# Optimization experiments

Measured on AMD Instinct MI355X. Metric: run time of the kernel, lower is better.

The kernel has to match this reference:

```python
import jax, jax.numpy as jnp
import numpy as np

EMBED = 1024
KEY = 64
HEAD = 64
CTX = 4096
BATCH = 8


def _linear(x, w, b):
    # torch nn.Linear: y = x @ W.T + b, W shape [out, in]
    return x @ w.T + b


def setup_inputs() -> dict:
    key = jax.random.key(0)
    ks = jax.random.split(key, 11)
    s_e = 1.0 / np.sqrt(EMBED)
    s_k = 1.0 / np.sqrt(KEY)
    return {
        "embeddings": jax.random.normal(ks[0], (BATCH, CTX, EMBED), dtype=jnp.float32),
        "kw1": jax.random.uniform(ks[1], (KEY, EMBED), jnp.float32, -s_e, s_e),
        "kb1": jax.random.uniform(ks[2], (KEY,), jnp.float32, -s_e, s_e),
        "kw2": jax.random.uniform(ks[3], (KEY, KEY), jnp.float32, -s_k, s_k),
        "kb2": jax.random.uniform(ks[4], (KEY,), jnp.float32, -s_k, s_k),
        "qw1": jax.random.uniform(ks[5], (KEY, EMBED), jnp.float32, -s_e, s_e),
        "qb1": jax.random.uniform(ks[6], (KEY,), jnp.float32, -s_e, s_e),
        "qw2": jax.random.uniform(ks[7], (KEY, KEY), jnp.float32, -s_k, s_k),
        "qb2": jax.random.uniform(ks[8], (KEY,), jnp.float32, -s_k, s_k),
        "vw": jax.random.uniform(ks[9], (HEAD, EMBED), jnp.float32, -s_e, s_e),
        "vb": jax.random.uniform(ks[10], (HEAD,), jnp.float32, -s_e, s_e),
    }


def reference(embeddings, kw1, kb1, kw2, kb2, qw1, qb1, qw2, qb2, vw, vb):
    T = embeddings.shape[1]
    keys = jax.nn.relu(_linear(jax.nn.relu(_linear(embeddings, kw1, kb1)), kw2, kb2))
    queries = jax.nn.relu(_linear(jax.nn.relu(_linear(embeddings, qw1, qb1)), qw2, qb2))
    values = _linear(embeddings, vw, vb)
    # scores: [B, T, T]
    scores = jnp.einsum("btk,bsk->bts", queries, keys) / np.sqrt(KEY).astype(np.float32)
    # Faithful to original: tril(ones) * -1e10 added (masks lower triangle incl. diagonal)
    mask = jnp.tril(jnp.ones((T, T), dtype=jnp.float32)) * jnp.float32(-1e10)
    weights = jax.nn.softmax(scores + mask, axis=-1)
    return jnp.einsum("bts,bsh->bth", weights, values)
```

## Files before the change

### kernel.cpp

```cpp
#include <hip/hip_runtime.h>
#include <hip/hip_bf16.h>
#include <math.h>

#define NB   8
#define TCTX 4096
#define ED   1024
#define KD   64

typedef __attribute__((ext_vector_type(8))) short bf16x8;
typedef __attribute__((ext_vector_type(4))) float f32x4;

#define LOG2E  1.44269504088896340736f
#define SCALE2 (0.125f * LOG2E)
#define MASK2  (-1e10f * LOG2E)

__device__ __forceinline__ void lds_fence() {
    asm volatile("s_waitcnt lgkmcnt(0)" ::: "memory");
    __builtin_amdgcn_sched_barrier(0);
}

__device__ __forceinline__ unsigned short f2bf(float f) {
    union { float f; unsigned u; } c; c.f = f;
    return (unsigned short)((c.u + 0x7FFFu + ((c.u >> 16) & 1u)) >> 16);
}
__device__ __forceinline__ int swz(int row, int byteoff) {
    return row * 128 + (byteoff ^ ((row & 7) << 4));
}
__device__ __forceinline__ f32x4 fzero4() {
    f32x4 z; z[0] = 0.f; z[1] = 0.f; z[2] = 0.f; z[3] = 0.f; return z;
}
__device__ __forceinline__ void gl_lds16(const void* g, void* l) {
    __builtin_amdgcn_global_load_lds(
        (const __attribute__((address_space(1))) unsigned int*)g,
        (__attribute__((address_space(3))) unsigned int*)l, 16, 0, 0);
}
__device__ __forceinline__ unsigned cvtpk_bf16(float lo, float hi) {
    unsigned r;
    asm("v_cvt_pk_bf16_f32 %0, %1, %2" : "=v"(r) : "v"(lo), "v"(hi));
    return r;
}

__global__ __launch_bounds__(256) void prep_kernel(
    const float* __restrict__ kw1, const float* __restrict__ qw1,
    const float* __restrict__ vw,  const float* __restrict__ kw2,
    const float* __restrict__ qw2,
    unsigned short* __restrict__ W1p, unsigned short* __restrict__ W2p)
{
    int idx = blockIdx.x * 256 + threadIdx.x;
    if (idx < 24576) {
        int ks = idx / 1536, rem = idx % 1536;
        int r = rem >> 3, bb = rem & 7;
        int c = bb ^ (r & 7);
        const float* src = (r < 64)  ? (kw1 + r * ED)
                         : (r < 128) ? (qw1 + (r - 64) * ED)
                                     : (vw  + (r - 128) * ED);
        src += ks * 64 + c * 8;
        unsigned short* dst = W1p + (size_t)idx * 8;
        #pragma unroll
        for (int e = 0; e < 8; ++e) dst[e] = f2bf(src[e]);
    } else if (idx < 25600) {
        int j = idx - 24576;
        int lane = j & 63, kh = (j >> 6) & 1, n = (j >> 7) & 3, kq = j >> 9;
        int row = n * 16 + (lane & 15);
        int ko  = kh * 32 + (lane >> 4) * 8;
        const float* src = (kq ? qw2 : kw2) + row * 64 + ko;
        unsigned short* dst = W2p + (size_t)j * 8;
        #pragma unroll
        for (int e = 0; e < 8; ++e) dst[e] = f2bf(src[e]);
    }
}

__global__ __launch_bounds__(256, 2) void proj_kernel(
    const float* __restrict__ emb,
    const unsigned short* __restrict__ W1p, const unsigned short* __restrict__ W2p,
    const float* __restrict__ kb1, const float* __restrict__ kb2,
    const float* __restrict__ qb1, const float* __restrict__ qb2,
    const float* __restrict__ vb,
    unsigned short* __restrict__ Qo, unsigned short* __restrict__ Ko,
    unsigned short* __restrict__ Vt)
{
    __shared__ __align__(16) char lds[80 * 1024];

    const int tid  = threadIdx.x;
    const int lane = tid & 63;
    const int w    = tid >> 6;
    const int lr   = lane & 15;
    const int lg   = lane >> 4;
    const long r0  = (long)blockIdx.x * 64;
    const int  b   = blockIdx.x >> 6;
    const int  tb  = (blockIdx.x & 63) * 64;

    const float* embB = emb + r0 * ED;

    f32x4 acc[12];
    #pragma unroll
    for (int j = 0; j < 12; ++j) acc[j] = fzero4();

    auto stageA = [&](int buf, int ks) {
        char* Abuf = lds + buf * 16 * 1024;
        const float* eb = embB + ks * 64;
        #pragma unroll
        for (int j = 0; j < 4; ++j) {
            int chunk = j * 4 + w;
            int r = chunk * 4 + (lane >> 4);
            int c = (lane & 15) ^ (r & 7);
            gl_lds16(eb + (long)r * ED + c * 4, Abuf + chunk * 1024);
        }
    };
    auto stageB = [&](int buf, int ks) {
        char* Bbuf = lds + 32 * 1024 + buf * 24 * 1024;
        const unsigned short* wb = W1p + (size_t)ks * 12288;
        #pragma unroll
        for (int j = 0; j < 6; ++j) {
            int chunk = j * 4 + w;
            gl_lds16(wb + chunk * 512 + lane * 8, Bbuf + chunk * 1024);
        }
    };

    stageA(0, 0); stageB(0, 0);
    __syncthreads();

    int cur = 0;
    for (int ks = 0; ks < 16; ++ks) {
        if (ks < 15) { stageA(cur ^ 1, ks + 1); stageB(cur ^ 1, ks + 1); }
        char* Ac = lds + cur * 16 * 1024;
        char* Bc = lds + 32 * 1024 + cur * 24 * 1024;
        const int r = w * 16 + lr;
        #pragma unroll
        for (int kh = 0; kh < 2; ++kh) {
            int cb0 = kh * 8 + lg * 2;
            float4 fa = *(const float4*)(Ac + r * 256 + ((cb0 ^ (r & 7)) * 16));
            float4 fb = *(const float4*)(Ac + r * 256 + (((cb0 + 1) ^ (r & 7)) * 16));
            bf16x8 a;
            a[0] = (short)f2bf(fa.x); a[1] = (short)f2bf(fa.y);
            a[2] = (short)f2bf(fa.z); a[3] = (short)f2bf(fa.w);
            a[4] = (short)f2bf(fb.x); a[5] = (short)f2bf(fb.y);
            a[6] = (short)f2bf(fb.z); a[7] = (short)f2bf(fb.w);
            #pragma unroll
            for (int n = 0; n < 12; ++n) {
                bf16x8 bv = *(const bf16x8*)(Bc + swz(n * 16 + lr, kh * 64 + lg * 16));
                acc[n] = __builtin_amdgcn_mfma_f32_16x16x32_bf16(a, bv, acc[n], 0, 0, 0);
            }
        }
        __syncthreads();
        cur ^= 1;
    }

    char* H  = lds + w * 2048;
    char* VT = lds + 16 * 1024;

    #pragma unroll
    for (int kq = 0; kq < 2; ++kq) {
        const float* b1 = kq ? qb1 : kb1;
        const float* b2 = kq ? qb2 : kb2;
        unsigned short* dst = kq ? Qo : Ko;
        const float oscale = kq ? SCALE2 : 1.0f;
        #pragma unroll
        for (int n = 0; n < 4; ++n) {
            int col = n * 16 + lr;
            float bias = b1[col];
            #pragma unroll
            for (int rr = 0; rr < 4; ++rr) {
                int row = lg * 4 + rr;
                *(unsigned short*)(H + swz(row, col * 2)) =
                    f2bf(fmaxf(acc[kq * 4 + n][rr] + bias, 0.f));
            }
        }
        lds_fence();
        bf16x8 a2k0 = *(const bf16x8*)(H + swz(lr, 0 * 64 + lg * 16));
        bf16x8 a2k1 = *(const bf16x8*)(H + swz(lr, 1 * 64 + lg * 16));
        lds_fence();

        f32x4 acc2[4];
        #pragma unroll
        for (int n = 0; n < 4; ++n) acc2[n] = fzero4();
        #pragma unroll
        for (int n = 0; n < 4; ++n) {
            bf16x8 w2f0 = *(const bf16x8*)(W2p + ((kq * 4 + n) * 2 + 0) * 512 + lane * 8);
            bf16x8 w2f1 = *(const bf16x8*)(W2p + ((kq * 4 + n) * 2 + 1) * 512 + lane * 8);
            acc2[n] = __builtin_amdgcn_mfma_f32_16x16x32_bf16(a2k0, w2f0, acc2[n], 0, 0, 0);
            acc2[n] = __builtin_amdgcn_mfma_f32_16x16x32_bf16(a2k1, w2f1, acc2[n], 0, 0, 0);
        }
        #pragma unroll
        for (int n = 0; n < 4; ++n) {
            int col = n * 16 + lr;
            float bias = b2[col];
            #pragma unroll
            for (int rr = 0; rr < 4; ++rr) {
                long rg = r0 + w * 16 + lg * 4 + rr;
                dst[rg * KD + col] = f2bf(fmaxf(acc2[n][rr] + bias, 0.f) * oscale);
            }
        }
    }

    #pragma unroll
    for (int n = 0; n < 4; ++n) {
        int col = n * 16 + lr;
        float bias = vb[col];
        #pragma unroll
        for (int rr = 0; rr < 4; ++rr) {
            int tl = w * 16 + lg * 4 + rr;
            *(unsigned short*)(VT + swz(col, tl * 2)) = f2bf(acc[8 + n][rr] + bias);
        }
    }
    __syncthreads();
    #pragma unroll
    for (int it = 0; it < 2; ++it) {
        int c = it * 256 + tid;
        int h = c >> 3, c4 = c & 7;
        *(int4*)(Vt + ((long)b * KD + h) * TCTX + tb + c4 * 8) =
            *(const int4*)(VT + swz(h, c4 * 16));
    }
}

__global__ __launch_bounds__(128) void attn_kernel(
    const unsigned short* __restrict__ Qb,
    const unsigned short* __restrict__ Kb,
    const unsigned short* __restrict__ Vt,
    float* __restrict__ Opart, float2* __restrict__ MSum)
{
    __shared__ __align__(16) char lds[20 * 1024];

    const int bid  = blockIdx.x;
    const int b    = bid & 7;
    const int half = (bid >> 3) & 1;
    const int qr   = bid >> 4;
    const int qi   = (qr + 127) & 127;
    const int t0   = qi * 32;
    const int tid = threadIdx.x, lane = tid & 63, w = tid >> 6;
    const int lr  = lane & 15, lg = lane >> 4;
    const int tg  = t0 + w * 16 + lr;

    char* Kl = lds;
    char* Vl = lds + 8 * 1024;
    char* QP = lds + 16 * 1024 + w * 2048;

    const unsigned short* Qg  = Qb + ((long)b * TCTX + t0 + w * 16) * KD;
    const unsigned short* Kg0 = Kb + (long)b * TCTX * KD;
    const unsigned short* Vg0 = Vt + (long)b * KD * TCTX;

    const int srow = lane >> 3;
    const int sblk = lane & 7;

    const int s0q = (qi == 127) ? 0 : (qi >> 1);
    const int len = 64 - s0q;
    const int mid = s0q + ((len + 1) >> 1);
    const int s_lo = half ? mid : s0q;
    const int s_hi = half ? 64  : mid;

    auto stageK = [&](int si) {
        const unsigned short* Kg = Kg0 + si * 64 * KD;
        #pragma unroll
        for (int j = 0; j < 4; ++j) {
            int chunk = w * 4 + j;
            int r = chunk * 8 + srow;
            int c = sblk ^ (r & 7);
            gl_lds16(Kg + r * KD + c * 8, Kl + chunk * 1024);
        }
    };
    auto stageV = [&](int si) {
        const unsigned short* Vg = Vg0 + si * 64;
        #pragma unroll
        for (int j = 0; j < 4; ++j) {
            int chunk = w * 4 + j;
            int r = chunk * 8 + srow;
            int c = sblk ^ (r & 7);
            gl_lds16(Vg + (long)r * TCTX + c * 8, Vl + chunk * 1024);
        }
    };

    float m2 = MASK2, sum_p = 0.f;
    f32x4 O[4];
    #pragma unroll
    for (int n = 0; n < 4; ++n) O[n] = fzero4();

    if (s_lo < s_hi) {
        #pragma unroll
        for (int j = 0; j < 2; ++j) {
            int r = j * 8 + srow;
            int c = sblk ^ (r & 7);
            gl_lds16(Qg + r * KD + c * 8, QP + j * 1024);
        }
        stageK(s_lo);
        stageV(s_lo);
        __syncthreads();

        bf16x8 qf[2];
        #pragma unroll
        for (int kh = 0; kh < 2; ++kh)
            qf[kh] = *(const bf16x8*)(QP + swz(lr, kh * 64 + lg * 16));

        for (int si = s_lo; si < s_hi; ++si) {
            f32x4 sc[4];
            #pragma unroll
            for (int mi = 0; mi < 4; ++mi) sc[mi] = fzero4();
            __builtin_amdgcn_s_setprio(1);
            #pragma unroll
            for (int kh = 0; kh < 2; ++kh) {
                #pragma unroll
                for (int mi = 0; mi < 4; ++mi) {
                    bf16x8 kf = *(const bf16x8*)(Kl + swz(mi * 16 + lr, kh * 64 + lg * 16));
                    sc[mi] = __builtin_amdgcn_mfma_f32_16x16x32_bf16(kf, qf[kh], sc[mi], 0, 0, 0);
                }
            }
            __builtin_amdgcn_s_setprio(0);

            __syncthreads();
            if (si + 1 < s_hi) stageK(si + 1);

            const int thr = tg - si * 64;
            float s2v[4][4];
            #pragma unroll
            for (int mi = 0; mi < 4; ++mi)
                #pragma unroll
                for (int rr = 0; rr < 4; ++rr) {
                    int sl = mi * 16 + lg * 4 + rr;
                    s2v[mi][rr] = (sl <= thr) ? MASK2 : sc[mi][rr];
                }

            float pml = s2v[0][0];
            #pragma unroll
            for (int mi = 0; mi < 4; ++mi)
                #pragma unroll
                for (int rr = 0; rr < 4; ++rr) pml = fmaxf(pml, s2v[mi][rr]);

            if (!__all(pml - m2 <= 8.0f)) {
                float pm = pml;
                pm = fmaxf(pm, __shfl_xor(pm, 16, 64));
                pm = fmaxf(pm, __shfl_xor(pm, 32, 64));
                float mnew = fmaxf(m2, pm);
                float scl = __builtin_amdgcn_exp2f(m2 - mnew);
                m2 = mnew;
                sum_p *= scl;
                #pragma unroll
                for (int rr = 0; rr < 4; ++rr) {
                    float sb = __shfl(scl, lg * 4 + rr, 64);
                    #pragma unroll
                    for (int n = 0; n < 4; ++n) O[n][rr] *= sb;
                }
            }
            float ls = 0.f;
            #pragma unroll
            for (int mi = 0; mi < 4; ++mi)
                #pragma unroll
                for (int rr = 0; rr < 4; ++rr) {
                    s2v[mi][rr] = __builtin_amdgcn_exp2f(s2v[mi][rr] - m2);
                    ls += s2v[mi][rr];
                }
            sum_p += ls;

            #pragma unroll
            for (int mi = 0; mi < 4; ++mi) {
                unsigned lo = cvtpk_bf16(s2v[mi][0], s2v[mi][1]);
                unsigned hi = cvtpk_bf16(s2v[mi][2], s2v[mi][3]);
                *(uint2*)(QP + swz(lr, mi * 32 + lg * 8)) = make_uint2(lo, hi);
            }
            lds_fence();
            bf16x8 ap0 = *(const bf16x8*)(QP + swz(lr, 0 * 64 + lg * 16));
            bf16x8 ap1 = *(const bf16x8*)(QP + swz(lr, 1 * 64 + lg * 16));
            lds_fence();

            __builtin_amdgcn_s_setprio(1);
            #pragma unroll
            for (int n = 0; n < 4; ++n) {
                bf16x8 bv0 = *(const bf16x8*)(Vl + swz(n * 16 + lr, 0 * 64 + lg * 16));
                bf16x8 bv1 = *(const bf16x8*)(Vl + swz(n * 16 + lr, 1 * 64 + lg * 16));
                O[n] = __builtin_amdgcn_mfma_f32_16x16x32_bf16(ap0, bv0, O[n], 0, 0, 0);
                O[n] = __builtin_amdgcn_mfma_f32_16x16x32_bf16(ap1, bv1, O[n], 0, 0, 0);
            }
            __builtin_amdgcn_s_setprio(0);

            __syncthreads();
            if (si + 1 < s_hi) stageV(si + 1);
        }
    }

    float sr = sum_p;
    sr += __shfl_xor(sr, 16, 64);
    sr += __shfl_xor(sr, 32, 64);
    const long rbase = (long)b * TCTX + t0 + w * 16;
    #pragma unroll
    for (int rr = 0; rr < 4; ++rr) {
        int tl = lg * 4 + rr;
        long rowi = (rbase + tl) * 2 + half;
        #pragma unroll
        for (int n = 0; n < 4; ++n)
            Opart[rowi * 64 + n * 16 + lr] = O[n][rr];
    }
    if (lg == 0)
        MSum[(rbase + lr) * 2 + half] = make_float2(m2, sr);
}

__global__ __launch_bounds__(256) void combine_kernel(
    const float* __restrict__ Opart, const float2* __restrict__ MSum,
    float* __restrict__ out)
{
    const long total = (long)NB * TCTX * KD;
    for (long idx = (long)blockIdx.x * 256 + threadIdx.x; idx < total;
         idx += (long)gridDim.x * 256) {
        long r = idx >> 6;
        int  h = (int)(idx & 63);
        float2 A = MSum[r * 2 + 0];
        float2 B = MSum[r * 2 + 1];
        float M  = fmaxf(A.x, B.x);
        float wa = __builtin_amdgcn_exp2f(A.x - M);
        float wb = __builtin_amdgcn_exp2f(B.x - M);
        float denom = A.y * wa + B.y * wb;
        float oa = Opart[(r * 2 + 0) * 64 + h];
        float ob = Opart[(r * 2 + 1) * 64 + h];
        out[idx] = (oa * wa + ob * wb) / denom;
    }
}

extern "C" void kernel_launch(void* const* d_in, const int* in_sizes, int n_in,
                              void* d_out, int out_size, void* d_ws, size_t ws_size,
                              hipStream_t stream) {
    const float* emb = (const float*)d_in[0];
    const float* kw1 = (const float*)d_in[1];
    const float* kb1 = (const float*)d_in[2];
    const float* kw2 = (const float*)d_in[3];
    const float* kb2 = (const float*)d_in[4];
    const float* qw1 = (const float*)d_in[5];
    const float* qb1 = (const float*)d_in[6];
    const float* qw2 = (const float*)d_in[7];
    const float* qb2 = (const float*)d_in[8];
    const float* vw  = (const float*)d_in[9];
    const float* vb  = (const float*)d_in[10];

    unsigned short* Qb  = (unsigned short*)d_ws;
    unsigned short* Kb  = Qb + (size_t)NB * TCTX * KD;
    unsigned short* Vt  = Kb + (size_t)NB * TCTX * KD;
    unsigned short* W1p = Vt + (size_t)NB * TCTX * KD;
    unsigned short* W2p = W1p + 196608;
    float*  Opart = (float*)(W2p + 8192);
    float2* MSum  = (float2*)(Opart + (size_t)NB * TCTX * 2 * KD);

    hipLaunchKernelGGL(prep_kernel, dim3(100), dim3(256), 0, stream,
                       kw1, qw1, vw, kw2, qw2, W1p, W2p);
    hipLaunchKernelGGL(proj_kernel, dim3(512), dim3(256), 0, stream,
                       emb, W1p, W2p, kb1, kb2, qb1, qb2, vb,
                       Qb, Kb, Vt);
    hipLaunchKernelGGL(attn_kernel, dim3(2048), dim3(128), 0, stream,
                       Qb, Kb, Vt, Opart, MSum);
    hipLaunchKernelGGL(combine_kernel, dim3(2048), dim3(256), 0, stream,
                       Opart, MSum, (float*)d_out);
}
```

Measured before the change: 84.98 us.

## Use 64-row query tiles with four-way key split and bf16 partial outputs

The attention kernel now gives each block 64 query rows and 4 waves instead of 32 rows and 2 waves, so each staged K/V tile is shared by more rows. The key range is split four ways instead of two, which keeps the block count while raising per-block reuse. Partial outputs are stored as bf16 to halve partial-result traffic, and the combine kernel merges four partials. The cost is more partial state to merge and reduced precision in the intermediate outputs. The diff is cut off, so it is unclear whether the Q staging and QP LDS layout were changed to handle 4 waves.

```diff
diff --git a/kernel.cpp b/kernel.cpp
--- a/kernel.cpp
+++ b/kernel.cpp
@@ -22,6 +22,9 @@
 __device__ __forceinline__ unsigned short f2bf(float f) {
     union { float f; unsigned u; } c; c.f = f;
     return (unsigned short)((c.u + 0x7FFFu + ((c.u >> 16) & 1u)) >> 16);
+}
+__device__ __forceinline__ float bf2f(unsigned short u) {
+    union { unsigned u; float f; } c; c.u = ((unsigned)u) << 16; return c.f;
 }
 __device__ __forceinline__ int swz(int row, int byteoff) {
     return row * 128 + (byteoff ^ ((row & 7) << 4));
@@ -213,20 +216,20 @@
     }
 }
 
-__global__ __launch_bounds__(128) void attn_kernel(
+__global__ __launch_bounds__(256) void attn_kernel(
     const unsigned short* __restrict__ Qb,
     const unsigned short* __restrict__ Kb,
     const unsigned short* __restrict__ Vt,
-    float* __restrict__ Opart, float2* __restrict__ MSum)
+    unsigned short* __restrict__ Opart, float2* __restrict__ MSum)
 {
-    __shared__ __align__(16) char lds[20 * 1024];
+    __shared__ __align__(16) char lds[24 * 1024];
 
     const int bid  = blockIdx.x;
     const int b    = bid & 7;
-    const int half = (bid >> 3) & 1;
-    const int qr   = bid >> 4;
-    const int qi   = (qr + 127) & 127;
-    const int t0   = qi * 32;
+    const int part = (bid >> 3) & 3;
+    const int qr   = bid >> 5;
+    const int qi   = (qr + 63) & 63;
+    const int t0   = qi * 64;
     const int tid = threadIdx.x, lane = tid & 63, w = tid >> 6;
     const int lr  = lane & 15, lg = lane >> 4;
     const int tg  = t0 + w * 16 + lr;
@@ -242,17 +245,16 @@
     const int srow = lane >> 3;
     const int sblk = lane & 7;
 
-    const int s0q = (qi == 127) ? 0 : (qi >> 1);
+    const int s0q = (qi == 63) ? 0 : qi;
     const int len = 64 - s0q;
-    const int mid = s0q + ((len + 1) >> 1);
-    const int s_lo = half ? mid : s0q;
-    const int s_hi = half ? 64  : mid;
+    const int s_lo = s0q + (len * part) / 4;
+    const int s_hi = s0q + (len * (part + 1)) / 4;
 
     auto stageK = [&](int si) {
         const unsigned short* Kg = Kg0 + si * 64 * KD;
         #pragma unroll
-        for (int j = 0; j < 4; ++j) {
-            int chunk = w * 4 + j;
+        for (int j = 0; j < 2; ++j) {
+            int chunk = w * 2 + j;
             int r = chunk * 8 + srow;
             int c = sblk ^ (r & 7);
             gl_lds16(Kg + r * KD + c * 8, Kl + chunk * 1024);
@@ -261,8 +263,8 @@
     auto stageV = [&](int si) {
         const unsigned short* Vg = Vg0 + si * 64;
         #pragma unroll
-        for (int j = 0; j < 4; ++j) {
-            int chunk = w * 4 + j;
+        for (int j = 0; j < 2; ++j) {
+            int chunk = w * 2 + j;
             int r = chunk * 8 + srow;
             int c = sblk ^ (r & 7);
             gl_lds16(Vg + (long)r * TCTX + c * 8, Vl + chunk * 1024);
@@ -382,17 +384,17 @@
     #pragma unroll
     for (int rr = 0; rr < 4; ++rr) {
         int tl = lg * 4 + rr;
-        long rowi = (rbase + tl) * 2 + half;
+        long rowi = (rbase + tl) * 4 + part;
         #pragma unroll
         for (int n = 0; n < 4; ++n)
-            Opart[rowi * 64 + n * 16 + lr] = O[n][rr];
+            Opart[rowi * 64 + n * 16 + lr] = f2bf(O[n][rr]);
     }
     if (lg == 0)
-        MSum[(rbase + lr) * 2 + half] = make_float2(m2, sr);
+        MSum[(rbase + lr) * 4 + part] = make_float2(m2, sr);
 }
 
 __global__ __launch_bounds__(256) void combine_kernel(
-    const float* __restrict__ Opart, const float2* __restrict__ MSum,
+    const unsigned short* __restrict__ Opart, const float2* __restrict__ MSum,
     float* __restrict__ out)
 {
     const long total = (long)NB * TCTX * KD;
@@ -400,15 +402,18 @@
          idx += (long)gridDim.x * 256) {
         long r = idx >> 6;
         int  h = (int)(idx & 63);
-        float2 A = MSum[r * 2 + 0];
-        float2 B = MSum[r * 2 + 1];
-        float M  = fmaxf(A.x, B.x);
-        float wa = __builtin_amdgcn_exp2f(A.x - M);
-        float wb = __builtin_amdgcn_exp2f(B.x - M);
-        float denom = A.y * wa + B.y * wb;
-        float oa = Opart[(r * 2 + 0) * 64 + h];
-        float ob = Opart[(r * 2 + 1) * 64 + h];
-        out[idx] = (oa * wa + ob * wb) / denom;
+        float2 ms[4];
+        #pragma unroll
+        for (int p = 0; p < 4; ++p) ms[p] = MSum[r * 4 + p];
+        float M = fmaxf(fmaxf(ms[0].x, ms[1].x), fmaxf(ms[2].x, ms[3].x));
+        float denom = 0.f, ov = 0.f;
+        #pragma unroll
+        for (int p = 0; p < 4; ++p) {
+            float wp = __builtin_amdgcn_exp2f(ms[p].x - M);
+            denom += ms[p].y * wp;
+            ov += bf2f(Opart[(r * 4 + p) * 64 + h]) * wp;
+        }
+        out[idx] = ov / denom;
     }
 }
 
@@ -432,15 +437,15 @@
     unsigned short* Vt  = Kb + (size_t)NB * TCTX * KD;
     unsigned short* W1p = Vt + (size_t)NB * TCTX * KD;
     unsigned short* W2p = W1p + 196608;
-    float*  Opart = (float*)(W2p + 8192);
-    float2* MSum  = (float2*)(Opart + (size_t)NB * TCTX * 2 * KD);
+    unsigned short* Opart = W2p + 8192;
+    float2* MSum = (float2*)(Opart + (size_t)NB * TCTX * 4 * KD);
 
     hipLaunchKernelGGL(prep_kernel, dim3(100), dim3(256), 0, stream,
                        kw1, qw1, vw, kw2, qw2, W1p, W2p);
     hipLaunchKernelGGL(proj_kernel, dim3(512), dim3(256), 0, stream,
                        emb, W1p, W2p, kb1, kb2, qb1, qb2, vb,
                        Qb, Kb, Vt);
-    hipLaunchKernelGGL(attn_kernel, dim3(2048), dim3(128), 0, stream,
+    hipLaunchKernelGGL(attn_kernel, dim3(2048), dim3(256), 0, stream,
                        Qb, Kb, Vt, Opart, MSum);
     hipLaunchKernelGGL(combine_kernel, dim3(2048), dim3(256), 0, stream,
                        Opart, MSum, (float*)d_out);
```

Result: faster. 79.57 us (-6.4%).
